# Optimization experiments

Hardware: AMD Instinct MI355X
Metric: run time of the kernel (lower is better)

The kernel has to match this reference:

```python
import jax, jax.numpy as jnp
import numpy as np

HIDDEN = 8   # TrajGRU hidden channels (hardcoded in module)
L = 5        # number of flow links
NEG = 0.2    # leaky relu slope (HKO-7 RNN_ACT_TYPE)


def conv2d(x, w, b, pad):
    y = jax.lax.conv_general_dilated(x, w, (1, 1), [(pad, pad), (pad, pad)],
                                     dimension_numbers=('NCHW', 'OIHW', 'NCHW'))
    return y + b[None, :, None, None]


def leaky(x):
    return jnp.where(x >= 0, x, NEG * x)


def bilinear_sample(im, x, y):
    # im: (C,H,W); x,y: (H,W) pixel coords; zero padding outside (grid_sample align_corners=True)
    C, H, W = im.shape
    x0 = jnp.floor(x); y0 = jnp.floor(y)
    wx = x - x0; wy = y - y0

    def g(ix, iy):
        valid = (ix >= 0) & (ix <= W - 1) & (iy >= 0) & (iy <= H - 1)
        ic = jnp.clip(ix, 0, W - 1).astype(jnp.int32)
        jc = jnp.clip(iy, 0, H - 1).astype(jnp.int32)
        return jnp.where(valid[None], im[:, jc, ic], 0.0)

    v00 = g(x0, y0); v01 = g(x0 + 1, y0)
    v10 = g(x0, y0 + 1); v11 = g(x0 + 1, y0 + 1)
    top = v00 * (1 - wx) + v01 * wx
    bot = v10 * (1 - wx) + v11 * wx
    return top * (1 - wy) + bot * wy


def trajgru_step(x, h, w_i2h, b_i2h, w_i2f, b_i2f, w_h2f, b_h2f,
                 w_flows, b_flows, w_ret, b_ret):
    B, C, H, W = h.shape
    # flow generator
    f = leaky(conv2d(x, w_i2f, b_i2f, 2) + conv2d(h, w_h2f, b_h2f, 2))
    flows = conv2d(f, w_flows, b_flows, 2).reshape(B, L, 2, H, W)
    # warp hidden along each link: wrap(h, -flow) => sample at grid - flow
    xx = jnp.arange(W, dtype=jnp.float32)[None, :] * jnp.ones((H, 1), jnp.float32)
    yy = jnp.arange(H, dtype=jnp.float32)[:, None] * jnp.ones((1, W), jnp.float32)
    cx = xx - flows[:, :, 0]  # (B,L,H,W)
    cy = yy - flows[:, :, 1]
    warp_b = jax.vmap(lambda hb, cxb, cyb:
                      jax.vmap(lambda a, b2: bilinear_sample(hb, a, b2))(cxb, cyb))
    warped = warp_b(h, cx, cy).reshape(B, L * C, H, W)  # (B, L*C, H, W)
    h2h = conv2d(warped, w_ret, b_ret, 0)
    i2h = conv2d(x, w_i2h, b_i2h, 1)
    i_r, i_u, i_m = jnp.split(i2h, 3, axis=1)
    h_r, h_u, h_m = jnp.split(h2h, 3, axis=1)
    reset = jax.nn.sigmoid(i_r + h_r)
    update = jax.nn.sigmoid(i_u + h_u)
    new_mem = leaky(i_m + reset * h_m)
    return update * h + (1.0 - update) * new_mem


def setup_inputs():
    key = jax.random.key(0)
    ks = jax.random.split(key, 16)
    B, T_in, T_out, H, W = 32, 12, 12, 128, 128
    in_ch = T_in + T_out
    p = lambda k, shape: 0.1 * jax.random.normal(k, shape, dtype=jnp.float32)
    return {
        'radar_data': jax.random.normal(ks[0], (B, T_in, 1, H, W), dtype=jnp.float32),
        'first_stage_pred': jax.random.normal(ks[1], (B, T_out, 1, H, W), dtype=jnp.float32),
        'w_conv_in': p(ks[2], (HIDDEN, in_ch, 3, 3)), 'b_conv_in': p(ks[3], (HIDDEN,)),
        'w_i2h': p(ks[4], (3 * HIDDEN, HIDDEN, 3, 3)), 'b_i2h': p(ks[5], (3 * HIDDEN,)),
        'w_i2f': p(ks[6], (32, HIDDEN, 5, 5)), 'b_i2f': p(ks[7], (32,)),
        'w_h2f': p(ks[8], (32, HIDDEN, 5, 5)), 'b_h2f': p(ks[9], (32,)),
        'w_flows': p(ks[10], (2 * L, 32, 5, 5)), 'b_flows': p(ks[11], (2 * L,)),
        'w_ret': p(ks[12], (3 * HIDDEN, L * HIDDEN, 1, 1)), 'b_ret': p(ks[13], (3 * HIDDEN,)),
        'w_conv_out': p(ks[14], (T_out, HIDDEN, 1, 1)), 'b_conv_out': p(ks[15], (T_out,)),
    }


def reference(radar_data, first_stage_pred, w_conv_in, b_conv_in, w_i2h, b_i2h,
              w_i2f, b_i2f, w_h2f, b_h2f, w_flows, b_flows, w_ret, b_ret,
              w_conv_out, b_conv_out):
    B, T_in, _, H, W = radar_data.shape
    T_out = first_stage_pred.shape[1]
    x = jnp.concatenate([radar_data.reshape(B, T_in, H, W),
                         first_stage_pred.reshape(B, T_out, H, W)], axis=1)
    x = conv2d(x, w_conv_in, b_conv_in, 1)          # (B, hidden, H, W)
    h0 = jnp.zeros((B, HIDDEN, H, W), x.dtype)       # TrajGRU zero initial state
    h = trajgru_step(x, h0, w_i2h, b_i2h, w_i2f, b_i2f, w_h2f, b_h2f,
                     w_flows, b_flows, w_ret, b_ret)  # seq_len == 1
    out = conv2d(h, w_conv_out, b_conv_out, 0)       # (B, pred_len, H, W)
    return out.reshape(B, T_out, 1, H, W)
```

## Files before the change

kernel.cpp:

```cpp
#include <hip/hip_runtime.h>
#include <hip/hip_bf16.h>


typedef __fp16   h2f __attribute__((ext_vector_type(2)));
typedef _Float16 v8h __attribute__((ext_vector_type(8)));
typedef float    v4f __attribute__((ext_vector_type(4)));

#define HW 128
#define SPITCH 24
#define PCOLS 36
#define NPOS  720
#define SXW   34
#define SXN   612

#define WB_HOFF 4608
#define FLT_OFF 16384
#define N_PREP  7828

__global__ __launch_bounds__(256)
void prep(const float* __restrict__ w_in,  const float* __restrict__ b_in,
          const float* __restrict__ w_i2h, const float* __restrict__ b_i2h,
          const float* __restrict__ b_ret, const float* __restrict__ w_out,
          const float* __restrict__ b_out, void* __restrict__ ws)
{
    int idx = blockIdx.x * 256 + threadIdx.x;
    _Float16* wh = (_Float16*)ws;
    float* fw = (float*)((char*)ws + FLT_OFF);
    if (idx < 4608) {
        int j = idx & 7, r = idx >> 3;
        int lane = r & 63, sg = r >> 6;
        int g = sg % 3, s = sg / 3;
        int quad = lane >> 4, n = lane & 15;
        int tap = s * 4 + quad;
        float v = (n < 8 && tap < 9) ? w_in[n*216 + (g*8 + j)*9 + tap] : 0.f;
        wh[idx] = (_Float16)v;
    } else if (idx < 7680) {
        int i2 = idx - 4608;
        int j = i2 & 7, r = i2 >> 3;
        int lane = r & 63; r >>= 6;
        int nt = r & 1, s = r >> 1;
        int quad = lane >> 4, n = lane & 15;
        int kk = s * 32 + quad * 8 + j;
        int t = kk >> 3, m = kk & 7;
        int o = nt * 16 + n;
        float v = (t < 9 && o < 24) ? w_i2h[o*72 + m*9 + t] : 0.f;
        wh[WB_HOFF + i2] = (_Float16)v;
    } else if (idx < N_PREP) {
        int j = idx - 7680;
        float v;
        if (j < 32) {
            int c = j & 7, sel = j >> 3;
            v = (sel==0) ? b_i2h[c]    + b_ret[c]
              : (sel==1) ? b_i2h[8+c]  + b_ret[8+c]
              : (sel==2) ? b_i2h[16+c] : b_ret[16+c];
        } else if (j < 128) v = w_out[j-32];
        else if (j < 140)   v = b_out[j-128];
        else                v = b_in[j-140];
        fw[j] = v;
    }
}

__device__ __forceinline__ void pack_store(_Float16* dst, const float* v)
{
    union { h2f h2[12]; v8h h8[3]; } u;
#pragma unroll
    for (int k = 0; k < 12; ++k)
        u.h2[k] = __builtin_amdgcn_cvt_pkrtz(v[2 * k], v[2 * k + 1]);
#pragma unroll
    for (int k = 0; k < 3; ++k) *(v8h*)&dst[8 * k] = u.h8[k];
}

__global__ __launch_bounds__(512, 8)
void radar2_mfma(const float* __restrict__ radar,
                 const float* __restrict__ pred,
                 const void*  __restrict__ ws,
                 float* __restrict__ out)
{
    __shared__ __align__(16) char pool[NPOS * SPITCH * 2];
    _Float16* s_in = (_Float16*)pool;
    _Float16* s_x  = (_Float16*)pool;
    float*    s_hc = (float*)(pool + 9792);

    const _Float16* wh = (const _Float16*)ws;
    const float* fw = (const float*)((const char*)ws + FLT_OFF);

    const int tid  = threadIdx.x;
    const int lane = tid & 63;
    const int wave = tid >> 6;
    const int quad = lane >> 4;
    const int col  = lane & 15;

    const int id   = blockIdx.x;
    const int b    = (id & 7) * 4 + (id >> 8);
    const int tile = (id >> 3) & 31;
    const int ty0  = (tile >> 2) << 4;
    const int tx0  = (tile & 3) << 5;

    const float* rb = radar + (((size_t)b * 12) << 14);
    const float* pb = pred  + (((size_t)b * 12) << 14);

    const int r0 = tid, r1 = tid + 512;
    const int ly0 = r0 / PCOLS, lx0 = r0 - PCOLS * ly0;
    const int gy0 = ty0 + ly0 - 2, gx0 = tx0 + lx0 - 2;
    const bool in0 = ((unsigned)gy0 < HW) & ((unsigned)gx0 < HW);
    const int off0 = (gy0 << 7) + gx0;
    const bool has1 = (r1 < NPOS);
    const int ly1 = r1 / PCOLS, lx1 = r1 - PCOLS * ly1;
    const int gy1 = ty0 + ly1 - 2, gx1 = tx0 + lx1 - 2;
    const bool in1 = has1 & ((unsigned)gy1 < HW) & ((unsigned)gx1 < HW);
    const int off1 = (gy1 << 7) + gx1;

    float va[24], vb24[24];
#pragma unroll
    for (int c = 0; c < 12; ++c) {
        va[c]      = in0 ? rb[((size_t)c << 14) + off0] : 0.f;
        va[12 + c] = in0 ? pb[((size_t)c << 14) + off0] : 0.f;
    }
#pragma unroll
    for (int c = 0; c < 12; ++c) {
        vb24[c]      = in1 ? rb[((size_t)c << 14) + off1] : 0.f;
        vb24[12 + c] = in1 ? pb[((size_t)c << 14) + off1] : 0.f;
    }
    pack_store(&s_in[r0 * SPITCH], va);
    if (has1) pack_store(&s_in[r1 * SPITCH], vb24);
    __syncthreads();

    int toffA[3];
#pragma unroll
    for (int s = 0; s < 3; ++s) {
        int t = s * 4 + quad;
        toffA[s] = (t < 9) ? ((t / 3) * PCOLS + (t % 3)) * SPITCH : 0;
    }
    int pbase[5];
#pragma unroll
    for (int t = 0; t < 5; ++t) {
        int p = (wave + 8 * t) * 16 + col; if (p > SXN - 1) p = SXN - 1;
        pbase[t] = ((p / SXW) * PCOLS + (p % SXW)) * SPITCH;
    }
    v4f accA[5];
#pragma unroll
    for (int t = 0; t < 5; ++t) accA[t] = (v4f){0.f, 0.f, 0.f, 0.f};
#pragma unroll
    for (int s = 0; s < 3; ++s) {
        v8h bg[3];
#pragma unroll
        for (int g = 0; g < 3; ++g)
            bg[g] = *(const v8h*)&wh[((s * 3 + g) * 64 + lane) * 8];
#pragma unroll
        for (int t = 0; t < 5; ++t) {
            if (wave + 8 * t < 39) {
                int ab = pbase[t] + toffA[s];
#pragma unroll
                for (int g = 0; g < 3; ++g) {
                    v8h a = *(const v8h*)&s_in[ab + g * 8];
                    accA[t] = __builtin_amdgcn_mfma_f32_16x16x32_f16(a, bg[g], accA[t], 0, 0, 0);
                }
            }
        }
    }
    __syncthreads();

    const float binv = fw[140 + (col & 7)];
    if (col < 8) {
#pragma unroll
        for (int t = 0; t < 5; ++t) {
            int mt = wave + 8 * t;
            if (mt < 39) {
#pragma unroll
                for (int r = 0; r < 4; ++r) {
                    int pa = mt * 16 + quad * 4 + r;
                    int py = pa / SXW, px = pa - SXW * py;
                    bool ok = ((unsigned)(ty0 + py - 1) < HW) &&
                              ((unsigned)(tx0 + px - 1) < HW);
                    if (pa < SXN)
                        s_x[pa * 8 + col] = (_Float16)(ok ? accA[t][r] + binv : 0.f);
                }
            }
        }
    }
    __syncthreads();

    int toff2[3];
#pragma unroll
    for (int s = 0; s < 3; ++s) {
        int t = s * 4 + quad;
        toff2[s] = (t < 9) ? ((t / 3) * SXW + (t % 3)) * 8 : 0;
    }
    int abase2[4];
#pragma unroll
    for (int t = 0; t < 4; ++t) {
        int q = (wave + 8 * t) * 16 + col;
        abase2[t] = ((q >> 5) * SXW + (q & 31)) * 8;
    }
    v4f acc0[4], acc1[4];
#pragma unroll
    for (int t = 0; t < 4; ++t) {
        acc0[t] = (v4f){0.f, 0.f, 0.f, 0.f};
        acc1[t] = (v4f){0.f, 0.f, 0.f, 0.f};
    }
#pragma unroll
    for (int s = 0; s < 3; ++s) {
        v8h b0 = *(const v8h*)&wh[WB_HOFF + ((s * 2 + 0) * 64 + lane) * 8];
        v8h b1 = *(const v8h*)&wh[WB_HOFF + ((s * 2 + 1) * 64 + lane) * 8];
#pragma unroll
        for (int t = 0; t < 4; ++t) {
            v8h a = *(const v8h*)&s_x[abase2[t] + toff2[s]];
            acc0[t] = __builtin_amdgcn_mfma_f32_16x16x32_f16(a, b0, acc0[t], 0, 0, 0);
            acc1[t] = __builtin_amdgcn_mfma_f32_16x16x32_f16(a, b1, acc1[t], 0, 0, 0);
        }
    }

    const int c7 = lane & 7;
    const float g0v = fw[c7], g1v = fw[8 + c7], g2v = fw[16 + c7], g3v = fw[24 + c7];
#pragma unroll
    for (int t = 0; t < 4; ++t) {
        int mt = wave + 8 * t;
#pragma unroll
        for (int r = 0; r < 4; ++r) {
            float iu = __shfl_xor(acc0[t][r], 8, 64);
            if (col < 8) {
                float rr = 1.f / (1.f + __expf(-(acc0[t][r] + g0v)));
                float uu = 1.f / (1.f + __expf(-(iu + g1v)));
                float mm = acc1[t][r] + g2v + rr * g3v;
                mm = (mm >= 0.f) ? mm : 0.2f * mm;
                s_hc[(mt * 16 + quad * 4 + r) * 9 + c7] = (1.f - uu) * mm;
            }
        }
    }
    __syncthreads();

    float h[8];
#pragma unroll
    for (int c = 0; c < 8; ++c) h[c] = s_hc[tid * 9 + c];
    const float* wout = fw + 32;
    const float* bout = fw + 128;
    const int oy = tid >> 5, ox = tid & 31;
    float* op = out + (((size_t)b * 12) << 14) + ((ty0 + oy) << 7) + (tx0 + ox);
#pragma unroll
    for (int t = 0; t < 12; ++t) {
        float o = bout[t];
#pragma unroll
        for (int c = 0; c < 8; ++c) o = fmaf(h[c], wout[t * 8 + c], o);
        op[(size_t)t << 14] = o;
    }
}

extern "C" void kernel_launch(void* const* d_in, const int* in_sizes, int n_in,
                              void* d_out, int out_size, void* d_ws, size_t ws_size,
                              hipStream_t stream) {
    (void)in_sizes; (void)n_in; (void)ws_size; (void)out_size;
    const float* radar = (const float*)d_in[0];
    const float* pred  = (const float*)d_in[1];
    const float* w_in  = (const float*)d_in[2];
    const float* b_in  = (const float*)d_in[3];
    const float* w_i2h = (const float*)d_in[4];
    const float* b_i2h = (const float*)d_in[5];
    const float* b_ret = (const float*)d_in[13];
    const float* w_out = (const float*)d_in[14];
    const float* b_out = (const float*)d_in[15];

    prep<<<(N_PREP + 255) / 256, 256, 0, stream>>>(w_in, b_in, w_i2h, b_i2h,
                                                   b_ret, w_out, b_out, d_ws);

    radar2_mfma<<<dim3(1024), dim3(512), 0, stream>>>(radar, pred, d_ws, (float*)d_out);
}
```

Baseline: 140.5 us.

## Process two tiles per block with double-buffered LDS prefetch of second tile

Each block now handles two adjacent 32-wide tiles using two LDS buffers. The global loads for the second tile are issued before computing the first tile, and their results are packed into the second buffer mid-way, hiding load latency behind MFMA work. The grid is halved and launch bounds drop to 4 waves per SIMD. Register pressure rises from holding 48 prefetched floats, and shared memory use roughly doubles, so occupancy falls.

```diff
diff --git a/kernel.cpp b/kernel.cpp
--- a/kernel.cpp
+++ b/kernel.cpp
@@ -12,6 +12,7 @@
 #define NPOS  720
 #define SXW   34
 #define SXN   612
+#define POOLB 34560
 
 #define WB_HOFF 4608
 #define FLT_OFF 16384
@@ -60,7 +61,7 @@
     }
 }
 
-__device__ __forceinline__ void pack_store(_Float16* dst, const float* v)
+__device__ __forceinline__ void pack24(_Float16* dst, const float* v)
 {
     union { h2f h2[12]; v8h h8[3]; } u;
 #pragma unroll
@@ -70,60 +71,13 @@
     for (int k = 0; k < 3; ++k) *(v8h*)&dst[8 * k] = u.h8[k];
 }
 
-__global__ __launch_bounds__(512, 8)
-void radar2_mfma(const float* __restrict__ radar,
-                 const float* __restrict__ pred,
-                 const void*  __restrict__ ws,
-                 float* __restrict__ out)
-{
-    __shared__ __align__(16) char pool[NPOS * SPITCH * 2];
+__device__ __forceinline__ void tile_front(char* pool, const _Float16* wh,
+    const float* fw, int lane, int wave, int quad, int col,
+    int ty0, int tx0)
+{
     _Float16* s_in = (_Float16*)pool;
     _Float16* s_x  = (_Float16*)pool;
     float*    s_hc = (float*)(pool + 9792);
-
-    const _Float16* wh = (const _Float16*)ws;
-    const float* fw = (const float*)((const char*)ws + FLT_OFF);
-
-    const int tid  = threadIdx.x;
-    const int lane = tid & 63;
-    const int wave = tid >> 6;
-    const int quad = lane >> 4;
-    const int col  = lane & 15;
-
-    const int id   = blockIdx.x;
-    const int b    = (id & 7) * 4 + (id >> 8);
-    const int tile = (id >> 3) & 31;
-    const int ty0  = (tile >> 2) << 4;
-    const int tx0  = (tile & 3) << 5;
-
-    const float* rb = radar + (((size_t)b * 12) << 14);
-    const float* pb = pred  + (((size_t)b * 12) << 14);
-
-    const int r0 = tid, r1 = tid + 512;
-    const int ly0 = r0 / PCOLS, lx0 = r0 - PCOLS * ly0;
-    const int gy0 = ty0 + ly0 - 2, gx0 = tx0 + lx0 - 2;
-    const bool in0 = ((unsigned)gy0 < HW) & ((unsigned)gx0 < HW);
-    const int off0 = (gy0 << 7) + gx0;
-    const bool has1 = (r1 < NPOS);
-    const int ly1 = r1 / PCOLS, lx1 = r1 - PCOLS * ly1;
-    const int gy1 = ty0 + ly1 - 2, gx1 = tx0 + lx1 - 2;
-    const bool in1 = has1 & ((unsigned)gy1 < HW) & ((unsigned)gx1 < HW);
-    const int off1 = (gy1 << 7) + gx1;
-
-    float va[24], vb24[24];
-#pragma unroll
-    for (int c = 0; c < 12; ++c) {
-        va[c]      = in0 ? rb[((size_t)c << 14) + off0] : 0.f;
-        va[12 + c] = in0 ? pb[((size_t)c << 14) + off0] : 0.f;
-    }
-#pragma unroll
-    for (int c = 0; c < 12; ++c) {
-        vb24[c]      = in1 ? rb[((size_t)c << 14) + off1] : 0.f;
-        vb24[12 + c] = in1 ? pb[((size_t)c << 14) + off1] : 0.f;
-    }
-    pack_store(&s_in[r0 * SPITCH], va);
-    if (has1) pack_store(&s_in[r1 * SPITCH], vb24);
-    __syncthreads();
 
     int toffA[3];
 #pragma unroll
@@ -227,8 +181,13 @@
             }
         }
     }
+}
+
+__device__ __forceinline__ void tile_back(char* pool, const float* fw,
+    int tid, int b, int ty0, int tx0, float* __restrict__ out)
+{
     __syncthreads();
-
+    float* s_hc = (float*)(pool + 9792);
     float h[8];
 #pragma unroll
     for (int c = 0; c < 8; ++c) h[c] = s_hc[tid * 9 + c];
@@ -243,6 +202,92 @@
         for (int c = 0; c < 8; ++c) o = fmaf(h[c], wout[t * 8 + c], o);
         op[(size_t)t << 14] = o;
     }
+}
+
+__global__ __launch_bounds__(512, 4)
+void radar2_mfma(const float* __restrict__ radar,
+                 const float* __restrict__ pred,
+                 const void*  __restrict__ ws,
+                 float* __restrict__ out)
+{
+    __shared__ __align__(16) char pool[2 * POOLB];
+    char* poolA = pool;
+    char* poolB = pool + POOLB;
+
+    const _Float16* wh = (const _Float16*)ws;
+    const float* fw = (const float*)((const char*)ws + FLT_OFF);
+
+    const int tid  = threadIdx.x;
+    const int lane = tid & 63;
+    const int wave = tid >> 6;
+    const int quad = lane >> 4;
+    const int col  = lane & 15;
+
+    const int id   = blockIdx.x;
+    const int b    = (id & 7) * 4 + (id >> 7);
+    const int bi   = (id >> 3) & 15;
+    const int ty0  = (bi >> 1) << 4;
+    const int tx0A = (bi & 1) << 6;
+    const int tx0B = tx0A + 32;
+
+    const float* rb = radar + (((size_t)b * 12) << 14);
+    const float* pb = pred  + (((size_t)b * 12) << 14);
+
+    const int r0 = tid, r1 = tid + 512;
+    const int ly0 = r0 / PCOLS, lx0 = r0 - PCOLS * ly0;
+    const int gy0 = ty0 + ly0 - 2;
+    const bool has1 = (r1 < NPOS);
+    const int ly1 = r1 / PCOLS, lx1 = r1 - PCOLS * ly1;
+    const int gy1 = ty0 + ly1 - 2;
+
+    const int gxA0 = tx0A + lx0 - 2, gxA1 = tx0A + lx1 - 2;
+    const int gxB0 = tx0B + lx0 - 2, gxB1 = tx0B + lx1 - 2;
+
+    const bool inA0 = ((unsigned)gy0 < HW) & ((unsigned)gxA0 < HW);
+    const bool inA1 = has1 & ((unsigned)gy1 < HW) & ((unsigned)gxA1 < HW);
+    const bool inB0 = ((unsigned)gy0 < HW) & ((unsigned)gxB0 < HW);
+    const bool inB1 = has1 & ((unsigned)gy1 < HW) & ((unsigned)gxB1 < HW);
+    const int offA0 = (gy0 << 7) + gxA0, offA1 = (gy1 << 7) + gxA1;
+    const int offB0 = (gy0 << 7) + gxB0, offB1 = (gy1 << 7) + gxB1;
+
+    {
+        float va[24], vb[24];
+#pragma unroll
+        for (int c = 0; c < 12; ++c) {
+            va[c]      = inA0 ? rb[((size_t)c << 14) + offA0] : 0.f;
+            va[12 + c] = inA0 ? pb[((size_t)c << 14) + offA0] : 0.f;
+        }
+#pragma unroll
+        for (int c = 0; c < 12; ++c) {
+            vb[c]      = inA1 ? rb[((size_t)c << 14) + offA1] : 0.f;
+            vb[12 + c] = inA1 ? pb[((size_t)c << 14) + offA1] : 0.f;
+        }
+        pack24(&((_Float16*)poolA)[r0 * SPITCH], va);
+        if (has1) pack24(&((_Float16*)poolA)[r1 * SPITCH], vb);
+    }
+    __syncthreads();
+
+    float vaB[24], vbB[24];
+#pragma unroll
+    for (int c = 0; c < 12; ++c) {
+        vaB[c]      = inB0 ? rb[((size_t)c << 14) + offB0] : 0.f;
+        vaB[12 + c] = inB0 ? pb[((size_t)c << 14) + offB0] : 0.f;
+    }
+#pragma unroll
+    for (int c = 0; c < 12; ++c) {
+        vbB[c]      = inB1 ? rb[((size_t)c << 14) + offB1] : 0.f;
+        vbB[12 + c] = inB1 ? pb[((size_t)c << 14) + offB1] : 0.f;
+    }
+
+    tile_front(poolA, wh, fw, lane, wave, quad, col, ty0, tx0A);
+
+    pack24(&((_Float16*)poolB)[r0 * SPITCH], vaB);
+    if (has1) pack24(&((_Float16*)poolB)[r1 * SPITCH], vbB);
+
+    tile_back(poolA, fw, tid, b, ty0, tx0A, out);
+
+    tile_front(poolB, wh, fw, lane, wave, quad, col, ty0, tx0B);
+    tile_back(poolB, fw, tid, b, ty0, tx0B, out);
 }
 
 extern "C" void kernel_launch(void* const* d_in, const int* in_sizes, int n_in,
@@ -262,5 +307,5 @@
     prep<<<(N_PREP + 255) / 256, 256, 0, stream>>>(w_in, b_in, w_i2h, b_i2h,
                                                    b_ret, w_out, b_out, d_ws);
 
-    radar2_mfma<<<dim3(1024), dim3(512), 0, stream>>>(radar, pred, d_ws, (float*)d_out);
-}
+    radar2_mfma<<<dim3(512), dim3(512), 0, stream>>>(radar, pred, d_ws, (float*)d_out);
+}
```

Result: slower. 150.9 us (+7.4%).
